# Kernel optimization log

Hardware: AMD Instinct MI355X
Metric: run time of the kernel (lower is better)

The kernel has to match this reference:

```python
import jax, jax.numpy as jnp
import numpy as np

B = 65536          # batch
H_DIM, W_DIM = 8, 8  # feather_size tuple
N = H_DIM * W_DIM    # 64 flat features
INNER = (N + 1) ** 2 # 4225 = outer-product size after prepending ones column
EPS = 1e-6


def setup_inputs() -> dict:
    key = jax.random.key(0)
    k1, k2 = jax.random.split(key, 2)
    x = jax.random.normal(k1, (B, N), jnp.float32)
    # nn.Linear(INNER, N): weight [out, in] = [N, INNER]
    W = jax.random.normal(k2, (N, INNER), jnp.float32) / np.sqrt(INNER)
    b = jnp.zeros((N,), jnp.float32)
    gamma = jnp.ones((N,), jnp.float32)   # LayerNorm scale
    beta = jnp.zeros((N,), jnp.float32)   # LayerNorm shift
    return {"x": x, "W": W, "b": b, "gamma": gamma, "beta": beta}


def reference(x, W, b, gamma, beta):
    Bsz = x.shape[0]
    # prepend ones column: [B, N+1]
    ones = jnp.ones((Bsz, 1), x.dtype)
    x1 = jnp.concatenate([ones, x], axis=-1)
    # bmm outer product x1 @ x1^T per row -> [B, N+1, N+1], flatten to [B, INNER]
    outer = (x1[:, :, None] * x1[:, None, :]).reshape(Bsz, INNER)
    # Linear(INNER -> N)
    y = outer @ W.T + b  # [B, N]
    # UER-py LayerNorm: gamma*(y-u)/sqrt(var+eps)+beta over last dim
    u = jnp.mean(y, axis=-1, keepdims=True)
    s = jnp.mean((y - u) ** 2, axis=-1, keepdims=True)
    y = gamma * (y - u) / jnp.sqrt(s + EPS) + beta
    # final view back to the (out) feather matrix shape
    return y.reshape(Bsz, H_DIM, W_DIM)
```

## Files before the change

kernel.cpp:

```cpp
#include <hip/hip_runtime.h>
#include <stdint.h>
#include <stddef.h>

typedef _Float16 f16;
typedef _Float16 f16x2 __attribute__((ext_vector_type(2)));
typedef _Float16 f16x4 __attribute__((ext_vector_type(4)));
typedef _Float16 f16x8 __attribute__((ext_vector_type(8)));
typedef float f32x16 __attribute__((ext_vector_type(16)));

#define INNER_SZ 4225
#define NQ 164
#define XSTR 72
#define NPH 41

__global__ __launch_bounds__(256) void cm_prep(const float* __restrict__ W,
                                               const float* __restrict__ bias,
                                               f16* __restrict__ Wf2,
                                               float* __restrict__ cvec) {
  int idx = blockIdx.x * 256 + threadIdx.x;
  if (idx < NQ * 1024) {
    int q   = idx >> 10;
    int r10 = idx & 1023;
    int ngh = r10 >> 9;
    int rr  = r10 & 511;
    int G   = rr >> 3;
    int e   = rr & 7;
    int c = G >> 1, hh = G & 1;
    int o = ngh * 32 + c;
    int kl = hh * 8 + e;
    float v = 0.f;
    if (q < 160) {
      int b, start;
      if (q < 16)      { b = 0; start = 0;  }
      else if (q < 48) { b = 1; start = 16; }
      else if (q < 96) { b = 2; start = 48; }
      else             { b = 3; start = 96; }
      int rel = q - start;
      int i = 16 * b + rel / (b + 1);
      int s = rel % (b + 1);
      int j = s * 16 + kl;
      if (j < i)
        v = W[o * INNER_SZ + (i + 1) * 65 + (j + 1)] +
            W[o * INNER_SZ + (j + 1) * 65 + (i + 1)];
      else if (j == i)
        v = W[o * INNER_SZ + (i + 1) * 65 + (i + 1)];
    } else {
      int j = (q - 160) * 16 + kl;
      v = W[o * INNER_SZ + (j + 1)] + W[o * INNER_SZ + (j + 1) * 65];
    }
    Wf2[idx] = (f16)v;
  }
  if (idx < 64) cvec[idx] = W[idx * INNER_SZ] + bias[idx];
}

__device__ inline void gload_lds16(const void* gp, void* lp) {
  __builtin_amdgcn_global_load_lds(
      (const __attribute__((address_space(1))) uint32_t*)(uintptr_t)gp,
      (__attribute__((address_space(3))) uint32_t*)(uintptr_t)lp, 16, 0, 0);
}

__device__ __forceinline__ f16x8 mulsp(f16x2 sp, f16x8 wv) {
  f16x8 r;
#pragma unroll
  for (int e = 0; e < 4; ++e)
    ((f16x2*)&r)[e] = sp * ((const f16x2*)&wv)[e];
  return r;
}

__global__ __launch_bounds__(256, 4) void cm_main(
    const float* __restrict__ x, const f16* __restrict__ Wf2,
    const float* __restrict__ cvec, const float* __restrict__ gamma,
    const float* __restrict__ beta, float* __restrict__ out) {
  __shared__ __align__(16) union SM {
    struct { f16 ring[2][4096]; f16 xs[128 * XSTR]; } k;
    float yt[8192];
  } sm;

  const int tid = threadIdx.x;
  const int lane = tid & 63;
  const int w = tid >> 6;
  const int rowg = w & 1;
  const int ch = w >> 1;
  const int c31 = lane & 31;
  const int h = lane >> 5;
  const long mbase = (long)blockIdx.x * 128;

  const char* wsrc = (const char*)Wf2 + lane * 16;
  char* ringb = (char*)&sm.k.ring[0][0];

#define STAGE2(P)                                                           \
  do {                                                                      \
    const char* s_ = wsrc + (size_t)(4 * (P) + w) * 2048;                   \
    char* d_ = ringb + (((P) & 1) ? 8192 : 0) + w * 2048;                   \
    gload_lds16(s_, d_);                                                    \
    gload_lds16(s_ + 1024, d_ + 1024);                                      \
  } while (0)

  STAGE2(0);

#pragma unroll
  for (int it = 0; it < 8; ++it) {
    int idx = it * 1024 + tid * 4;
    int row = idx >> 6, col = idx & 63;
    const float4 v = *(const float4*)(x + (size_t)(mbase + row) * 64 + col);
    f16x4 hv = {(f16)v.x, (f16)v.y, (f16)v.z, (f16)v.w};
    *(f16x4*)(sm.k.xs + row * XSTR + col) = hv;
  }
  __syncthreads();

  const int r0 = rowg * 64 + c31, r1 = rowg * 64 + 32 + c31;
  f16x8 xw0[4], xw1[4];
#pragma unroll
  for (int s = 0; s < 4; ++s) {
    xw0[s] = *(const f16x8*)(sm.k.xs + r0 * XSTR + s * 16 + h * 8);
    xw1[s] = *(const f16x8*)(sm.k.xs + r1 * XSTR + s * 16 + h * 8);
  }
#pragma unroll
  for (int s = 0; s < 4; ++s)
    asm volatile("" : "+v"(xw0[s]), "+v"(xw1[s]));

  const int bfo = ch * 1024 + (2 * c31 + h) * 16;

  f32x16 acc0 = (f32x16)(0.0f);
  f32x16 acc1 = (f32x16)(0.0f);
  uint32_t un0 = *(const uint16_t*)(sm.k.xs + r0 * XSTR);
  uint32_t un1 = *(const uint16_t*)(sm.k.xs + r1 * XSTR);
  f16x2 sp0 = {}, sp1 = {};

#pragma unroll
  for (int p = 0; p < NPH; ++p) {
    if (p + 1 < NPH) STAGE2(p + 1);
    const char* rb = ringb + ((p & 1) ? 8192 : 0);
#pragma unroll
    for (int kk = 0; kk < 4; ++kk) {
      const int q = 4 * p + kk;
      int i, s, lin;
      if (q >= 160) { i = 64; s = q - 160; lin = 1; }
      else {
        int b = (q < 16) ? 0 : (q < 48) ? 1 : (q < 96) ? 2 : 3;
        int st = (b == 0) ? 0 : (b == 1) ? 16 : (b == 2) ? 48 : 96;
        int rel = q - st;
        i = 16 * b + rel / (b + 1);
        s = rel % (b + 1);
        lin = 0;
      }
      bool newi;
      if (q == 0) newi = true;
      else if (lin) newi = false;
      else {
        int qp = q - 1;
        int bp = (qp < 16) ? 0 : (qp < 48) ? 1 : (qp < 96) ? 2 : 3;
        int stp = (bp == 0) ? 0 : (bp == 1) ? 16 : (bp == 2) ? 48 : 96;
        newi = (16 * bp + (qp - stp) / (bp + 1)) != i;
      }
      if (newi) {
        uint32_t u0 = un0 & 0xffffu, u1 = un1 & 0xffffu;
        sp0 = __builtin_bit_cast(f16x2, u0 | (u0 << 16));
        sp1 = __builtin_bit_cast(f16x2, u1 | (u1 << 16));
        if (i + 1 < 64) {
          un0 = *(const uint16_t*)(sm.k.xs + r0 * XSTR + i + 1);
          un1 = *(const uint16_t*)(sm.k.xs + r1 * XSTR + i + 1);
        }
      }
      f16x8 bf = *(const f16x8*)(rb + kk * 2048 + bfo);
      f16x8 a0, a1;
      if (lin) { a0 = xw0[s]; a1 = xw1[s]; }
      else     { a0 = mulsp(sp0, xw0[s]); a1 = mulsp(sp1, xw1[s]); }
      acc0 = __builtin_amdgcn_mfma_f32_32x32x16_f16(a0, bf, acc0, 0, 0, 0);
      acc1 = __builtin_amdgcn_mfma_f32_32x32x16_f16(a1, bf, acc1, 0, 0, 0);
    }
    __syncthreads();
  }

  {
    const int cg = ch * 32 + c31;
    const int swz = (c31 & 7) << 4;
#pragma unroll
    for (int rq = 0; rq < 4; ++rq) {
      int b0 = cg * 512 + rowg * 256 + 0 * 128 + rq * 32 + h * 16;
      int b1 = cg * 512 + rowg * 256 + 1 * 128 + rq * 32 + h * 16;
      *(float4*)((char*)sm.yt + (b0 ^ swz)) =
          make_float4(acc0[rq * 4 + 0], acc0[rq * 4 + 1], acc0[rq * 4 + 2], acc0[rq * 4 + 3]);
      *(float4*)((char*)sm.yt + (b1 ^ swz)) =
          make_float4(acc1[rq * 4 + 0], acc1[rq * 4 + 1], acc1[rq * 4 + 2], acc1[rq * 4 + 3]);
    }
  }
  __syncthreads();

  {
    int row = tid >> 1, half = tid & 1;
    float y[32];
    float s = 0.f, qs = 0.f;
#pragma unroll
    for (int j = 0; j < 32; ++j) {
      int c = half * 32 + j;
      int byte = (c * 512 + row * 4) ^ ((c & 7) << 4);
      float v = *(const float*)((const char*)sm.yt + byte);
      v += cvec[c];
      y[j] = v;
      s += v; qs += v * v;
    }
    s  += __shfl_xor(s, 1);
    qs += __shfl_xor(qs, 1);
    float mean = s * 0.015625f;
    float var = qs * 0.015625f - mean * mean;
    float rstd = rsqrtf(var + 1e-6f);
#pragma unroll
    for (int j = 0; j < 32; ++j) {
      int c = half * 32 + j;
      y[j] = gamma[c] * (y[j] - mean) * rstd + beta[c];
    }
    float* op = out + (size_t)(mbase + row) * 64 + half * 32;
#pragma unroll
    for (int j4 = 0; j4 < 8; ++j4)
      *(float4*)(op + j4 * 4) =
          make_float4(y[j4 * 4 + 0], y[j4 * 4 + 1], y[j4 * 4 + 2], y[j4 * 4 + 3]);
  }
#undef STAGE2
}

extern "C" void kernel_launch(void* const* d_in, const int* in_sizes, int n_in,
                              void* d_out, int out_size, void* d_ws, size_t ws_size,
                              hipStream_t stream) {
  const float* x     = (const float*)d_in[0];
  const float* W     = (const float*)d_in[1];
  const float* bias  = (const float*)d_in[2];
  const float* gamma = (const float*)d_in[3];
  const float* beta  = (const float*)d_in[4];
  float* out = (float*)d_out;

  f16* Wf2 = (f16*)d_ws;
  float* cvec = (float*)((char*)d_ws + NQ * 1024 * 2);

  cm_prep<<<(NQ * 1024 + 255) / 256, 256, 0, stream>>>(W, bias, Wf2, cvec);
  cm_main<<<512, 256, 0, stream>>>(x, Wf2, cvec, gamma, beta, out);
}
```

Measured before the change: 39.57 us.

## Double waves per block, triple-buffer W ring with waitcnt-based single barrier

```diff
diff --git a/kernel.cpp b/kernel.cpp
--- a/kernel.cpp
+++ b/kernel.cpp
@@ -67,20 +67,20 @@
   return r;
 }
 
-__global__ __launch_bounds__(256, 4) void cm_main(
+__global__ __launch_bounds__(512, 4) void cm_main(
     const float* __restrict__ x, const f16* __restrict__ Wf2,
     const float* __restrict__ cvec, const float* __restrict__ gamma,
     const float* __restrict__ beta, float* __restrict__ out) {
   __shared__ __align__(16) union SM {
-    struct { f16 ring[2][4096]; f16 xs[128 * XSTR]; } k;
+    struct { f16 ring[3][4096]; f16 xs[128 * XSTR]; } k;
     float yt[8192];
   } sm;
 
   const int tid = threadIdx.x;
   const int lane = tid & 63;
   const int w = tid >> 6;
-  const int rowg = w & 1;
-  const int ch = w >> 1;
+  const int rowg = w & 3;
+  const int ch = w >> 2;
   const int c31 = lane & 31;
   const int h = lane >> 5;
   const long mbase = (long)blockIdx.x * 128;
@@ -88,19 +88,16 @@
   const char* wsrc = (const char*)Wf2 + lane * 16;
   char* ringb = (char*)&sm.k.ring[0][0];
 
-#define STAGE2(P)                                                           \
-  do {                                                                      \
-    const char* s_ = wsrc + (size_t)(4 * (P) + w) * 2048;                   \
-    char* d_ = ringb + (((P) & 1) ? 8192 : 0) + w * 2048;                   \
-    gload_lds16(s_, d_);                                                    \
-    gload_lds16(s_ + 1024, d_ + 1024);                                      \
-  } while (0)
-
-  STAGE2(0);
-
-#pragma unroll
-  for (int it = 0; it < 8; ++it) {
-    int idx = it * 1024 + tid * 4;
+#define STAGE(P)                                                            \
+  gload_lds16(wsrc + (size_t)(4 * (P) + (w >> 1)) * 2048 + (w & 1) * 1024,  \
+              ringb + ((P) % 3) * 8192 + w * 1024)
+
+  STAGE(0);
+  STAGE(1);
+
+#pragma unroll
+  for (int it = 0; it < 4; ++it) {
+    int idx = it * 2048 + tid * 4;
     int row = idx >> 6, col = idx & 63;
     const float4 v = *(const float4*)(x + (size_t)(mbase + row) * 64 + col);
     f16x4 hv = {(f16)v.x, (f16)v.y, (f16)v.z, (f16)v.w};
@@ -108,29 +105,31 @@
   }
   __syncthreads();
 
-  const int r0 = rowg * 64 + c31, r1 = rowg * 64 + 32 + c31;
-  f16x8 xw0[4], xw1[4];
-#pragma unroll
-  for (int s = 0; s < 4; ++s) {
-    xw0[s] = *(const f16x8*)(sm.k.xs + r0 * XSTR + s * 16 + h * 8);
-    xw1[s] = *(const f16x8*)(sm.k.xs + r1 * XSTR + s * 16 + h * 8);
-  }
+  const int r0 = rowg * 32 + c31;
+  f16x8 xw[4];
 #pragma unroll
   for (int s = 0; s < 4; ++s)
-    asm volatile("" : "+v"(xw0[s]), "+v"(xw1[s]));
+    xw[s] = *(const f16x8*)(sm.k.xs + r0 * XSTR + s * 16 + h * 8);
+#pragma unroll
+  for (int s = 0; s < 4; ++s)
+    asm volatile("" : "+v"(xw[s]));
 
   const int bfo = ch * 1024 + (2 * c31 + h) * 16;
 
-  f32x16 acc0 = (f32x16)(0.0f);
-  f32x16 acc1 = (f32x16)(0.0f);
-  uint32_t un0 = *(const uint16_t*)(sm.k.xs + r0 * XSTR);
-  uint32_t un1 = *(const uint16_t*)(sm.k.xs + r1 * XSTR);
-  f16x2 sp0 = {}, sp1 = {};
+  f32x16 acc = (f32x16)(0.0f);
+  uint32_t un = *(const uint16_t*)(sm.k.xs + r0 * XSTR);
+  f16x2 sp = {};
 
 #pragma unroll
   for (int p = 0; p < NPH; ++p) {
-    if (p + 1 < NPH) STAGE2(p + 1);
-    const char* rb = ringb + ((p & 1) ? 8192 : 0);
+    if (p < NPH - 1) asm volatile("s_waitcnt vmcnt(1)" ::: "memory");
+    else             asm volatile("s_waitcnt vmcnt(0)" ::: "memory");
+    __builtin_amdgcn_s_barrier();
+    asm volatile("" ::: "memory");
+    __builtin_amdgcn_sched_barrier(0);
+    if (p + 2 < NPH) STAGE(p + 2);
+    const char* rb = ringb + (p % 3) * 8192;
+    __builtin_amdgcn_s_setprio(1);
 #pragma unroll
     for (int kk = 0; kk < 4; ++kk) {
       const int q = 4 * p + kk;
@@ -154,40 +153,32 @@
         newi = (16 * bp + (qp - stp) / (bp + 1)) != i;
       }
       if (newi) {
-        uint32_t u0 = un0 & 0xffffu, u1 = un1 & 0xffffu;
-        sp0 = __builtin_bit_cast(f16x2, u0 | (u0 << 16));
-        sp1 = __builtin_bit_cast(f16x2, u1 | (u1 << 16));
-        if (i + 1 < 64) {
-          un0 = *(const uint16_t*)(sm.k.xs + r0 * XSTR + i + 1);
-          un1 = *(const uint16_t*)(sm.k.xs + r1 * XSTR + i + 1);
-        }
+        uint32_t u = un & 0xffffu;
+        sp = __builtin_bit_cast(f16x2, u | (u << 16));
+        if (i + 1 < 64)
+          un = *(const uint16_t*)(sm.k.xs + r0 * XSTR + i + 1);
       }
       f16x8 bf = *(const f16x8*)(rb + kk * 2048 + bfo);
-      f16x8 a0, a1;
-      if (lin) { a0 = xw0[s]; a1 = xw1[s]; }
-      else     { a0 = mulsp(sp0, xw0[s]); a1 = mulsp(sp1, xw1[s]); }
-      acc0 = __builtin_amdgcn_mfma_f32_32x32x16_f16(a0, bf, acc0, 0, 0, 0);
-      acc1 = __builtin_amdgcn_mfma_f32_32x32x16_f16(a1, bf, acc1, 0, 0, 0);
-    }
-    __syncthreads();
-  }
-
+      f16x8 a = lin ? xw[s] : mulsp(sp, xw[s]);
+      acc = __builtin_amdgcn_mfma_f32_32x32x16_f16(a, bf, acc, 0, 0, 0);
+    }
+    __builtin_amdgcn_s_setprio(0);
+  }
+
+  __syncthreads();
   {
     const int cg = ch * 32 + c31;
     const int swz = (c31 & 7) << 4;
 #pragma unroll
     for (int rq = 0; rq < 4; ++rq) {
-      int b0 = cg * 512 + rowg * 256 + 0 * 128 + rq * 32 + h * 16;
-      int b1 = cg * 512 + rowg * 256 + 1 * 128 + rq * 32 + h * 16;
+      int b0 = cg * 512 + rowg * 128 + rq * 32 + h * 16;
       *(float4*)((char*)sm.yt + (b0 ^ swz)) =
-          make_float4(acc0[rq * 4 + 0], acc0[rq * 4 + 1], acc0[rq * 4 + 2], acc0[rq * 4 + 3]);
-      *(float4*)((char*)sm.yt + (b1 ^ swz)) =
-          make_float4(acc1[rq * 4 + 0], acc1[rq * 4 + 1], acc1[rq * 4 + 2], acc1[rq * 4 + 3]);
+          make_float4(acc[rq * 4 + 0], acc[rq * 4 + 1], acc[rq * 4 + 2], acc[rq * 4 + 3]);
     }
   }
   __syncthreads();
 
-  {
+  if (tid < 256) {
     int row = tid >> 1, half = tid & 1;
     float y[32];
     float s = 0.f, qs = 0.f;
@@ -216,7 +207,7 @@
       *(float4*)(op + j4 * 4) =
           make_float4(y[j4 * 4 + 0], y[j4 * 4 + 1], y[j4 * 4 + 2], y[j4 * 4 + 3]);
   }
-#undef STAGE2
+#undef STAGE
 }
 
 extern "C" void kernel_launch(void* const* d_in, const int* in_sizes, int n_in,
@@ -233,5 +224,5 @@
   float* cvec = (float*)((char*)d_ws + NQ * 1024 * 2);
 
   cm_prep<<<(NQ * 1024 + 255) / 256, 256, 0, stream>>>(W, bias, Wf2, cvec);
-  cm_main<<<512, 256, 0, stream>>>(x, Wf2, cvec, gamma, beta, out);
-}
+  cm_main<<<512, 512, 0, stream>>>(x, Wf2, cvec, gamma, beta, out);
+}
```

Measured after the change: 40.78 us. 3.1% more time.
